# Kernel tuning notes

Hardware: AMD Instinct MI355X
Metric: run time of the kernel (lower is better)

The kernel has to match this reference:

```python
import jax, jax.numpy as jnp
import numpy as np

B, N, E = 8, 1024, 512
H, D = 8, 64
F = 2048


def setup_inputs() -> dict:
    key = jax.random.key(0)
    ks = jax.random.split(key, 12)
    s = lambda *sh: 1.0 / np.sqrt(sh[-1])
    inp = {
        "input1": jax.random.normal(ks[0], (B, N, E), dtype=jnp.float32),
        # projection weights stored as [in, out] (torch weight transposed)
        "Wq": jax.random.normal(ks[1], (E, H * D), dtype=jnp.float32) * s(E, E),
        "Wk": jax.random.normal(ks[2], (E, H * D), dtype=jnp.float32) * s(E, E),
        "Wv": jax.random.normal(ks[3], (E, H * D), dtype=jnp.float32) * s(E, E),
        "Wo": jax.random.normal(ks[4], (H * D, E), dtype=jnp.float32) * s(E, E),
        "bo": jnp.zeros((E,), dtype=jnp.float32),
        "g1": jnp.ones((E,), dtype=jnp.float32),
        "b1": jnp.zeros((E,), dtype=jnp.float32),
        "W1": jax.random.normal(ks[5], (E, F), dtype=jnp.float32) * s(E, E),
        "bf1": jnp.zeros((F,), dtype=jnp.float32),
        "W2": jax.random.normal(ks[6], (F, E), dtype=jnp.float32) * s(F, F),
        "bf2": jnp.zeros((E,), dtype=jnp.float32),
        "g2": jnp.ones((E,), dtype=jnp.float32),
        "b2": jnp.zeros((E,), dtype=jnp.float32),
    }
    return inp


def _layernorm(x, g, b, eps=1e-5):
    mu = jnp.mean(x, axis=-1, keepdims=True)
    var = jnp.var(x, axis=-1, keepdims=True)
    return (x - mu) * jax.lax.rsqrt(var + eps) * g + b


def reference(input1, Wq, Wk, Wv, Wo, bo, g1, b1, W1, bf1, W2, bf2, g2, b2):
    x = input1
    # QKV projections, split heads: [B, H, N, D]
    q = (x @ Wq).reshape(B, N, H, D).transpose(0, 2, 1, 3)
    k = (x @ Wk).reshape(B, N, H, D).transpose(0, 2, 1, 3)
    v = (x @ Wv).reshape(B, N, H, D).transpose(0, 2, 1, 3)
    # scaled dot-product attention (naive, materialized scores as in source)
    score = jnp.einsum("bhnd,bhmd->bhnm", q, k) / jnp.sqrt(jnp.float32(D))
    weights = jax.nn.softmax(score, axis=-1)
    out = jnp.einsum("bhnm,bhmd->bhnd", weights, v)
    out_concat = out.transpose(0, 2, 1, 3).reshape(B, N, H * D)
    mh = out_concat @ Wo + bo
    out1 = _layernorm(x + mh, g1, b1)
    ff = jax.nn.relu(out1 @ W1 + bf1) @ W2 + bf2
    out3 = _layernorm(out1 + ff, g2, b2)
    return (out3, 0)
```

## Files before the change

kernel.cpp:

```cpp
#include <hip/hip_runtime.h>
#include <cstdint>
#include <cstddef>

typedef _Float16 h8 __attribute__((ext_vector_type(8)));
typedef _Float16 h4 __attribute__((ext_vector_type(4)));
typedef __fp16   g2 __attribute__((ext_vector_type(2)));
typedef float    f32x4 __attribute__((ext_vector_type(4)));

constexpr int B_ = 8, N_ = 1024, E_ = 512, H_ = 8, D_ = 64, F_ = 2048;
constexpr int M_ = B_ * N_;
constexpr int HD_ = H_ * D_;

#define QSCALE2 0.18033688011112042f

#define GLOAD_LDS16(gp, lp)                                                        \
    __builtin_amdgcn_global_load_lds((const __attribute__((address_space(1))) void*)(gp), \
                                     (__attribute__((address_space(3))) void*)(lp), 16, 0, 0)

__device__ __forceinline__ float exp2_raw(float x) {
#if __has_builtin(__builtin_amdgcn_exp2f)
    return __builtin_amdgcn_exp2f(x);
#else
    float r;
    asm("v_exp_f32 %0, %1\n\ts_nop 0" : "=v"(r) : "v"(x));
    return r;
#endif
}

__global__ void __launch_bounds__(256) k_pre(
    const float* __restrict__ x, _Float16* __restrict__ xh,
    const float* __restrict__ Wq, const float* __restrict__ Wk,
    const float* __restrict__ Wv, const float* __restrict__ Wo,
    const float* __restrict__ W1, const float* __restrict__ W2,
    _Float16* __restrict__ oqkv, _Float16* __restrict__ oo,
    _Float16* __restrict__ o1, _Float16* __restrict__ o2) {
    if (blockIdx.z == 12) {
        int i = (blockIdx.x * 256 + threadIdx.x) * 16;
#pragma unroll
        for (int j = 0; j < 4; ++j) {
            float4 v = *(const float4*)(x + i + j * 4);
            h4 o = {(_Float16)v.x, (_Float16)v.y, (_Float16)v.z, (_Float16)v.w};
            *(h4*)(xh + i + j * 4) = o;
        }
        return;
    }
    if (blockIdx.x >= 256) return;
    const float* in;
    _Float16* out;
    int R, C, gt = blockIdx.x;
    switch (blockIdx.z) {
        case 0: in = Wq; out = oqkv;              R = 512;  C = 512;  break;
        case 1: in = Wk; out = oqkv + 512 * 512;  R = 512;  C = 512;  break;
        case 2: in = Wv; out = oqkv + 1024 * 512; R = 512;  C = 512;  break;
        case 3: in = Wo; out = oo;                R = 512;  C = 512;  break;
        default:
            if (blockIdx.z < 8) { in = W1; out = o1; R = 512;  C = 2048; gt += (blockIdx.z - 4) * 256; }
            else                { in = W2; out = o2; R = 2048; C = 512;  gt += (blockIdx.z - 8) * 256; }
    }
    const int ctiles = C >> 5;
    const int ty = gt / ctiles, tx = gt - ty * ctiles;
    const int r0 = ty * 32, c0 = tx * 32;
    __shared__ float lt[32][33];
    const int rr = threadIdx.x >> 3, cq = threadIdx.x & 7;
    float4 v = *(const float4*)&in[(size_t)(r0 + rr) * C + c0 + cq * 4];
    lt[rr][cq * 4 + 0] = v.x; lt[rr][cq * 4 + 1] = v.y;
    lt[rr][cq * 4 + 2] = v.z; lt[rr][cq * 4 + 3] = v.w;
    __syncthreads();
    h4 o = {(_Float16)lt[cq * 4 + 0][rr], (_Float16)lt[cq * 4 + 1][rr],
            (_Float16)lt[cq * 4 + 2][rr], (_Float16)lt[cq * 4 + 3][rr]};
    *(h4*)&out[(size_t)(c0 + rr) * R + r0 + cq * 4] = o;
}

template <int BN, int EPI>
__global__ void __launch_bounds__(256) k_gemm(
    const _Float16* __restrict__ A, const _Float16* __restrict__ Bt,
    int Mg, int Ng, int Kg,
    const float* __restrict__ bias,
    const _Float16* __restrict__ resh, _Float16* __restrict__ outh,
    _Float16* __restrict__ qp, _Float16* __restrict__ kp, _Float16* __restrict__ vtp) {
    constexpr int WN = BN / 2;
    constexpr int NI = WN / 16;
    __shared__ alignas(16) _Float16 lA[2][64 * 64];
    __shared__ alignas(16) _Float16 lB[2][BN * 64];

    const int tid = threadIdx.x;
    const int lane = tid & 63;
    const int wid = tid >> 6;
    const int wr = wid >> 1, wc = wid & 1;
    const int r16 = lane & 15, hseg = lane >> 4;

    const int bid = blockIdx.x;
    const int xcd = bid & 7;
    const int rem = bid >> 3;
    const int tx = rem >> 4, tyl = rem & 15;
    const int m0 = (xcd * 16 + tyl) * 64;
    const int n0 = tx * BN;

    auto STAGE = [&](int buf, int k0) {
#pragma unroll
        for (int i = 0; i < 2; ++i) {
            const int slot = i * 256 + tid, row = slot >> 3;
            const int cs = (slot & 7) ^ (row & 7);
            GLOAD_LDS16(A + (size_t)(m0 + row) * Kg + k0 + cs * 8, &lA[buf][slot * 8]);
        }
#pragma unroll
        for (int i = 0; i < BN / 32; ++i) {
            const int slot = i * 256 + tid, row = slot >> 3;
            const int cs = (slot & 7) ^ (row & 7);
            GLOAD_LDS16(Bt + (size_t)(n0 + row) * Kg + k0 + cs * 8, &lB[buf][slot * 8]);
        }
    };

    f32x4 acc[2][NI] = {};
    const int nt = Kg >> 6;

    STAGE(0, 0);
    __syncthreads();

    for (int t = 0; t < nt; ++t) {
        const int cur = t & 1;
        if (t + 1 < nt) STAGE(cur ^ 1, (t + 1) << 6);

#pragma unroll
        for (int kk = 0; kk < 2; ++kk) {
            h8 af[2], bf[NI];
#pragma unroll
            for (int mi = 0; mi < 2; ++mi) {
                const int row = wr * 32 + mi * 16 + r16;
                af[mi] = *(const h8*)&lA[cur][row * 64 + (((kk * 4 + hseg) ^ (row & 7)) * 8)];
            }
#pragma unroll
            for (int ni = 0; ni < NI; ++ni) {
                const int row = wc * WN + ni * 16 + r16;
                bf[ni] = *(const h8*)&lB[cur][row * 64 + (((kk * 4 + hseg) ^ (row & 7)) * 8)];
            }
#pragma unroll
            for (int mi = 0; mi < 2; ++mi)
#pragma unroll
                for (int ni = 0; ni < NI; ++ni)
                    acc[mi][ni] =
                        __builtin_amdgcn_mfma_f32_16x16x32_f16(af[mi], bf[ni], acc[mi][ni], 0, 0, 0);
        }
        __syncthreads();
    }

    if constexpr (EPI == 0) {
        if (n0 >= 1024) {
            _Float16* lC = &lA[0][0];
#pragma unroll
            for (int mi = 0; mi < 2; ++mi) {
                const int r0 = wr * 32 + mi * 16 + hseg * 4;
                const int s = r0 >> 3, ro = r0 & 7;
#pragma unroll
                for (int ni = 0; ni < NI; ++ni) {
                    const int c = wc * WN + ni * 16 + r16;
                    h4 pv = {(_Float16)acc[mi][ni][0], (_Float16)acc[mi][ni][1],
                             (_Float16)acc[mi][ni][2], (_Float16)acc[mi][ni][3]};
                    *(h4*)&lC[c * 64 + ((s ^ (c & 7)) << 3) + ro] = pv;
                }
            }
            __syncthreads();
            const int c = tid >> 1, half = tid & 1;
            const int b = m0 >> 10, nn0 = m0 & 1023;
            _Float16* gdst =
                vtp + ((size_t)(b * 512 + (n0 - 1024) + c)) * 1024 + nn0 + half * 32;
#pragma unroll
            for (int j = 0; j < 4; ++j) {
                const int s = half * 4 + j;
                h8 v = *(const h8*)&lC[c * 64 + ((s ^ (c & 7)) << 3)];
                *(h8*)&gdst[j * 8] = v;
            }
        } else {
#pragma unroll
            for (int mi = 0; mi < 2; ++mi)
#pragma unroll
                for (int ni = 0; ni < NI; ++ni)
#pragma unroll
                    for (int r = 0; r < 4; ++r) {
                        int row = m0 + wr * 32 + mi * 16 + hseg * 4 + r;
                        int col = n0 + wc * WN + ni * 16 + r16;
                        float v = acc[mi][ni][r];
                        int cc = col & 511;
                        int h = cc >> 6, d = cc & 63;
                        int b = row >> 10, nn = row & 1023;
                        if (col < 512)
                            qp[((b * 8 + h) * 1024 + nn) * 64 + d] = (_Float16)(v * QSCALE2);
                        else
                            kp[((b * 8 + h) * 1024 + nn) * 64 + d] = (_Float16)v;
                    }
        }
    } else {
#pragma unroll
        for (int mi = 0; mi < 2; ++mi)
#pragma unroll
            for (int ni = 0; ni < NI; ++ni)
#pragma unroll
                for (int r = 0; r < 4; ++r) {
                    int row = m0 + wr * 32 + mi * 16 + hseg * 4 + r;
                    int col = n0 + wc * WN + ni * 16 + r16;
                    float v = acc[mi][ni][r] + bias[col];
                    if constexpr (EPI == 3) {
                        v += (float)resh[(size_t)row * Ng + col];
                    } else {
                        v = v > 0.f ? v : 0.f;
                    }
                    outh[(size_t)row * Ng + col] = (_Float16)v;
                }
    }
}

__global__ void __launch_bounds__(512) k_attn(const _Float16* __restrict__ q,
                                              const _Float16* __restrict__ k,
                                              const _Float16* __restrict__ vt,
                                              _Float16* __restrict__ attn) {
    __shared__ alignas(16) _Float16 lK[2][64 * 64];
    __shared__ alignas(16) _Float16 lV[2][64 * 64];
    __shared__ alignas(16) _Float16 lP[8][16 * 64];

    const int tid = threadIdx.x, lane = tid & 63, w = tid >> 6;
    const int bid = blockIdx.x;
    const int xcd = bid & 7, rem = bid >> 3;
    const int bh = xcd * 8 + (rem & 7);
    const int q0 = (rem >> 3) * 128;
    const int r16 = lane & 15, hseg = lane >> 4;
    const size_t base = (size_t)bh * N_ * D_;

    h8 qf0 = *(const h8*)&q[base + (size_t)(q0 + w * 16 + r16) * 64 + hseg * 8];
    h8 qf1 = *(const h8*)&q[base + (size_t)(q0 + w * 16 + r16) * 64 + 32 + hseg * 8];

    const int srow = tid >> 3;
    const int scsrc = (tid & 7) ^ (srow & 7);

    auto STAGE = [&](int buf, int kt) {
        GLOAD_LDS16(k + base + kt * 4096 + srow * 64 + scsrc * 8, &lK[buf][tid * 8]);
        GLOAD_LDS16(vt + base + (size_t)srow * N_ + kt * 64 + scsrc * 8, &lV[buf][tid * 8]);
    };

    float mrun = -1e30f, lrun = 0.f;
    f32x4 oacc[4] = {};

    const char* lKb = (const char*)&lK[0][0];
    const char* lVb = (const char*)&lV[0][0];
    char* lPb = (char*)&lP[0][0] + w * 2048;
    const int swz = r16 & 7;
    const int kb0 = r16 * 128 + ((hseg ^ swz) * 16);
    const int kb1 = r16 * 128 + (((4 + hseg) ^ swz) * 16);
    const int pswz = swz * 8;
    const int prd0 = r16 * 128 + (((hseg * 8) ^ pswz) * 2);
    const int prd1 = r16 * 128 + (((32 + hseg * 8) ^ pswz) * 2);
    const int pwr0 = r16 * 128 + (((0 + hseg * 4) ^ pswz) * 2);
    const int pwr1 = r16 * 128 + (((16 + hseg * 4) ^ pswz) * 2);
    const int pwr2 = r16 * 128 + (((32 + hseg * 4) ^ pswz) * 2);
    const int pwr3 = r16 * 128 + (((48 + hseg * 4) ^ pswz) * 2);

    auto TILE = [&](const int cur, const int kt) __attribute__((always_inline)) {
        if (kt + 1 < N_ / 64) STAGE(cur ^ 1, kt + 1);
        const int cOff = cur * 8192;

        float sv[4][4];
        __builtin_amdgcn_s_setprio(1);
#pragma unroll
        for (int t4 = 0; t4 < 4; ++t4) {
            f32x4 a = {};
            h8 kf0 = *(const h8*)(lKb + cOff + t4 * 2048 + kb0);
            a = __builtin_amdgcn_mfma_f32_16x16x32_f16(kf0, qf0, a, 0, 0, 0);
            h8 kf1 = *(const h8*)(lKb + cOff + t4 * 2048 + kb1);
            a = __builtin_amdgcn_mfma_f32_16x16x32_f16(kf1, qf1, a, 0, 0, 0);
#pragma unroll
            for (int r = 0; r < 4; ++r) sv[t4][r] = a[r];
        }
        __builtin_amdgcn_s_setprio(0);

        float m0a = fmaxf(fmaxf(sv[0][0], sv[0][1]), fmaxf(sv[0][2], sv[0][3]));
        float m1a = fmaxf(fmaxf(sv[1][0], sv[1][1]), fmaxf(sv[1][2], sv[1][3]));
        float m2a = fmaxf(fmaxf(sv[2][0], sv[2][1]), fmaxf(sv[2][2], sv[2][3]));
        float m3a = fmaxf(fmaxf(sv[3][0], sv[3][1]), fmaxf(sv[3][2], sv[3][3]));
        float mx = fmaxf(fmaxf(m0a, m1a), fmaxf(m2a, m3a));

        if (__any(mx > mrun + 8.f)) {
            mx = fmaxf(mx, __shfl_xor(mx, 16));
            mx = fmaxf(mx, __shfl_xor(mx, 32));
            float mnew = fmaxf(mrun, mx);
            float sc = exp2_raw(mrun - mnew);
            mrun = mnew;
            lrun *= sc;
#pragma unroll
            for (int r = 0; r < 4; ++r) {
                float scq = __shfl(sc, hseg * 4 + r);
#pragma unroll
                for (int nf = 0; nf < 4; ++nf) oacc[nf][r] *= scq;
            }
        }

        float p[4][4];
        float rsum = 0.f;
#pragma unroll
        for (int t4 = 0; t4 < 4; ++t4)
#pragma unroll
            for (int r = 0; r < 4; ++r) {
                p[t4][r] = exp2_raw(sv[t4][r] - mrun);
                rsum += p[t4][r];
            }
        lrun += rsum;

#pragma unroll
        for (int t4 = 0; t4 < 4; ++t4) {
            g2 a0 = __builtin_amdgcn_cvt_pkrtz(p[t4][0], p[t4][1]);
            g2 a1 = __builtin_amdgcn_cvt_pkrtz(p[t4][2], p[t4][3]);
            h4 pv = {(_Float16)a0[0], (_Float16)a0[1], (_Float16)a1[0], (_Float16)a1[1]};
            char* dst = lPb + (t4 == 0 ? pwr0 : t4 == 1 ? pwr1 : t4 == 2 ? pwr2 : pwr3);
            *(h4*)dst = pv;
        }
        asm volatile("s_waitcnt lgkmcnt(0)" ::: "memory");

        h8 pa0 = *(const h8*)(lPb + prd0);
        h8 pa1 = *(const h8*)(lPb + prd1);
        __builtin_amdgcn_s_setprio(1);
#pragma unroll
        for (int nf = 0; nf < 4; ++nf) {
            h8 vb0 = *(const h8*)(lVb + cOff + nf * 2048 + kb0);
            oacc[nf] = __builtin_amdgcn_mfma_f32_16x16x32_f16(pa0, vb0, oacc[nf], 0, 0, 0);
            h8 vb1 = *(const h8*)(lVb + cOff + nf * 2048 + kb1);
            oacc[nf] = __builtin_amdgcn_mfma_f32_16x16x32_f16(pa1, vb1, oacc[nf], 0, 0, 0);
        }
        __builtin_amdgcn_s_setprio(0);
        __syncthreads();
    };

    STAGE(0, 0);
    __syncthreads();

    for (int kt = 0; kt < N_ / 64; kt += 2) {
        TILE(0, kt);
        TILE(1, kt + 1);
    }

    lrun += __shfl_xor(lrun, 16);
    lrun += __shfl_xor(lrun, 32);

    float rlin = 1.f / lrun;
    int b = bh >> 3, h = bh & 7;
#pragma unroll
    for (int r = 0; r < 4; ++r) {
        float inv = __shfl(rlin, hseg * 4 + r);
        int row = b * 1024 + q0 + w * 16 + hseg * 4 + r;
#pragma unroll
        for (int nf = 0; nf < 4; ++nf) {
            int col = h * 64 + nf * 16 + r16;
            attn[(size_t)row * 512 + col] = (_Float16)(oacc[nf][r] * inv);
        }
    }
}

template <int OUTF32>
__global__ void __launch_bounds__(256) k_ln(const _Float16* __restrict__ x,
                                            const float* __restrict__ g,
                                            const float* __restrict__ b,
                                            float* __restrict__ outf,
                                            _Float16* __restrict__ outh,
                                            float* __restrict__ tail) {
    int row = blockIdx.x * 4 + (threadIdx.x >> 6);
    int lane = threadIdx.x & 63;
    h8 v = *(const h8*)(x + (size_t)row * 512 + lane * 8);
    float f[8];
    float s = 0.f, sq = 0.f;
#pragma unroll
    for (int j = 0; j < 8; ++j) {
        f[j] = (float)v[j];
        s += f[j];
        sq += f[j] * f[j];
    }
#pragma unroll
    for (int msk = 1; msk < 64; msk <<= 1) {
        s += __shfl_xor(s, msk);
        sq += __shfl_xor(sq, msk);
    }
    float mu = s * (1.f / 512.f);
    float var = sq * (1.f / 512.f) - mu * mu;
    float rstd = rsqrtf(var + 1e-5f);
    float4 ga = *(const float4*)(g + lane * 8);
    float4 gb = *(const float4*)(g + lane * 8 + 4);
    float4 ba = *(const float4*)(b + lane * 8);
    float4 bb = *(const float4*)(b + lane * 8 + 4);
    float o[8];
    o[0] = (f[0] - mu) * rstd * ga.x + ba.x;
    o[1] = (f[1] - mu) * rstd * ga.y + ba.y;
    o[2] = (f[2] - mu) * rstd * ga.z + ba.z;
    o[3] = (f[3] - mu) * rstd * ga.w + ba.w;
    o[4] = (f[4] - mu) * rstd * gb.x + bb.x;
    o[5] = (f[5] - mu) * rstd * gb.y + bb.y;
    o[6] = (f[6] - mu) * rstd * gb.z + bb.z;
    o[7] = (f[7] - mu) * rstd * gb.w + bb.w;
    if constexpr (OUTF32) {
        float* orow = outf + (size_t)row * 512 + lane * 8;
        *(float4*)(orow) = make_float4(o[0], o[1], o[2], o[3]);
        *(float4*)(orow + 4) = make_float4(o[4], o[5], o[6], o[7]);
        if (tail && blockIdx.x == 0 && threadIdx.x == 0) tail[0] = 0.f;
    } else {
        h8 oh = {(_Float16)o[0], (_Float16)o[1], (_Float16)o[2], (_Float16)o[3],
                 (_Float16)o[4], (_Float16)o[5], (_Float16)o[6], (_Float16)o[7]};
        *(h8*)(outh + (size_t)row * 512 + lane * 8) = oh;
    }
}

extern "C" void kernel_launch(void* const* d_in, const int* in_sizes, int n_in,
                              void* d_out, int out_size, void* d_ws, size_t ws_size,
                              hipStream_t stream) {
    const float* x   = (const float*)d_in[0];
    const float* Wq  = (const float*)d_in[1];
    const float* Wk  = (const float*)d_in[2];
    const float* Wv  = (const float*)d_in[3];
    const float* Wo  = (const float*)d_in[4];
    const float* bo  = (const float*)d_in[5];
    const float* g1  = (const float*)d_in[6];
    const float* b1  = (const float*)d_in[7];
    const float* W1  = (const float*)d_in[8];
    const float* bf1 = (const float*)d_in[9];
    const float* W2  = (const float*)d_in[10];
    const float* bf2 = (const float*)d_in[11];
    const float* g2  = (const float*)d_in[12];
    const float* b2  = (const float*)d_in[13];
    float* out = (float*)d_out;

    char* ws = (char*)d_ws;
    _Float16* xh    = (_Float16*)(ws + 0);
    _Float16* wqkvT = (_Float16*)(ws + 8388608);
    _Float16* woT   = (_Float16*)(ws + 9961472);
    _Float16* w1T   = (_Float16*)(ws + 10485760);
    _Float16* w2T   = (_Float16*)(ws + 12582912);
    _Float16* qb    = (_Float16*)(ws + 14680064);
    _Float16* kb    = (_Float16*)(ws + 23068672);
    _Float16* vtb   = (_Float16*)(ws + 31457280);
    _Float16* attnb = (_Float16*)(ws + 39845888);
    _Float16* h1h   = (_Float16*)(ws + 48234496);
    _Float16* out1h = xh;
    _Float16* ff    = qb;

    k_pre<<<dim3(1024, 1, 13), 256, 0, stream>>>(x, xh, Wq, Wk, Wv, Wo, W1, W2,
                                                 wqkvT, woT, w1T, w2T);

    k_gemm<128, 0><<<dim3(1536), 256, 0, stream>>>(
        xh, wqkvT, M_, 1536, 512, nullptr, nullptr, nullptr, qb, kb, vtb);

    k_attn<<<dim3(512), 512, 0, stream>>>(qb, kb, vtb, attnb);

    k_gemm<64, 3><<<dim3(1024), 256, 0, stream>>>(
        attnb, woT, M_, 512, 512, bo, xh, h1h, nullptr, nullptr, nullptr);

    k_ln<0><<<dim3(M_ / 4), 256, 0, stream>>>(h1h, g1, b1, nullptr, out1h, nullptr);

    k_gemm<128, 2><<<dim3(2048), 256, 0, stream>>>(
        out1h, w1T, M_, 2048, 512, bf1, nullptr, ff, nullptr, nullptr, nullptr);

    k_gemm<64, 3><<<dim3(1024), 256, 0, stream>>>(
        ff, w2T, M_, 512, 2048, bf2, out1h, h1h, nullptr, nullptr, nullptr);

    k_ln<1><<<dim3(M_ / 4), 256, 0, stream>>>(h1h, g2, b2, out, nullptr, out + (size_t)M_ * E_);
}
```

Measured before the change: 144.4 us.

## Add dedicated 128x64-tile GEMM with 8 waves for N=512 residual GEMMs

```diff
diff --git a/kernel.cpp b/kernel.cpp
--- a/kernel.cpp
+++ b/kernel.cpp
@@ -71,13 +71,14 @@
     *(h4*)&out[(size_t)(c0 + rr) * R + r0 + cq * 4] = o;
 }
 
-template <int BN, int EPI>
+template <int EPI>
 __global__ void __launch_bounds__(256) k_gemm(
     const _Float16* __restrict__ A, const _Float16* __restrict__ Bt,
     int Mg, int Ng, int Kg,
     const float* __restrict__ bias,
-    const _Float16* __restrict__ resh, _Float16* __restrict__ outh,
+    _Float16* __restrict__ outh,
     _Float16* __restrict__ qp, _Float16* __restrict__ kp, _Float16* __restrict__ vtp) {
+    constexpr int BN = 128;
     constexpr int WN = BN / 2;
     constexpr int NI = WN / 16;
     __shared__ alignas(16) _Float16 lA[2][64 * 64];
@@ -199,14 +200,92 @@
                     int row = m0 + wr * 32 + mi * 16 + hseg * 4 + r;
                     int col = n0 + wc * WN + ni * 16 + r16;
                     float v = acc[mi][ni][r] + bias[col];
-                    if constexpr (EPI == 3) {
-                        v += (float)resh[(size_t)row * Ng + col];
-                    } else {
-                        v = v > 0.f ? v : 0.f;
-                    }
+                    v = v > 0.f ? v : 0.f;
                     outh[(size_t)row * Ng + col] = (_Float16)v;
                 }
     }
+}
+
+__global__ void __launch_bounds__(512) k_gemm64(
+    const _Float16* __restrict__ A, const _Float16* __restrict__ Bt,
+    int Ng, int Kg,
+    const float* __restrict__ bias,
+    const _Float16* __restrict__ resh, _Float16* __restrict__ outh) {
+    __shared__ alignas(16) _Float16 lA[2][128 * 64];
+    __shared__ alignas(16) _Float16 lB[2][64 * 64];
+
+    const int tid = threadIdx.x;
+    const int lane = tid & 63;
+    const int wid = tid >> 6;
+    const int wr = wid >> 1;
+    const int wc = wid & 1;
+    const int r16 = lane & 15, hseg = lane >> 4;
+
+    const int bid = blockIdx.x;
+    const int xcd = bid & 7;
+    const int rem = bid >> 3;
+    const int tx = rem >> 3, tyl = rem & 7;
+    const int m0 = (xcd * 8 + tyl) * 128;
+    const int n0 = tx * 64;
+
+    auto STAGE = [&](int buf, int k0) {
+#pragma unroll
+        for (int i = 0; i < 2; ++i) {
+            const int slot = i * 512 + tid, row = slot >> 3;
+            const int cs = (slot & 7) ^ (row & 7);
+            GLOAD_LDS16(A + (size_t)(m0 + row) * Kg + k0 + cs * 8, &lA[buf][slot * 8]);
+        }
+        {
+            const int slot = tid, row = slot >> 3;
+            const int cs = (slot & 7) ^ (row & 7);
+            GLOAD_LDS16(Bt + (size_t)(n0 + row) * Kg + k0 + cs * 8, &lB[buf][slot * 8]);
+        }
+    };
+
+    f32x4 acc[2][2] = {};
+    const int nt = Kg >> 6;
+
+    STAGE(0, 0);
+    __syncthreads();
+
+    for (int t = 0; t < nt; ++t) {
+        const int cur = t & 1;
+        if (t + 1 < nt) STAGE(cur ^ 1, (t + 1) << 6);
+
+#pragma unroll
+        for (int kk = 0; kk < 2; ++kk) {
+            h8 af[2], bf[2];
+#pragma unroll
+            for (int mi = 0; mi < 2; ++mi) {
+                const int row = wr * 32 + mi * 16 + r16;
+                af[mi] = *(const h8*)&lA[cur][row * 64 + (((kk * 4 + hseg) ^ (row & 7)) * 8)];
+            }
+#pragma unroll
+            for (int ni = 0; ni < 2; ++ni) {
+                const int row = wc * 32 + ni * 16 + r16;
+                bf[ni] = *(const h8*)&lB[cur][row * 64 + (((kk * 4 + hseg) ^ (row & 7)) * 8)];
+            }
+#pragma unroll
+            for (int mi = 0; mi < 2; ++mi)
+#pragma unroll
+                for (int ni = 0; ni < 2; ++ni)
+                    acc[mi][ni] =
+                        __builtin_amdgcn_mfma_f32_16x16x32_f16(af[mi], bf[ni], acc[mi][ni], 0, 0, 0);
+        }
+        __syncthreads();
+    }
+
+#pragma unroll
+    for (int mi = 0; mi < 2; ++mi)
+#pragma unroll
+        for (int ni = 0; ni < 2; ++ni)
+#pragma unroll
+            for (int r = 0; r < 4; ++r) {
+                int row = m0 + wr * 32 + mi * 16 + hseg * 4 + r;
+                int col = n0 + wc * 32 + ni * 16 + r16;
+                float v = acc[mi][ni][r] + bias[col] + (float)resh[(size_t)row * Ng + col];
+                outh[(size_t)row * Ng + col] = (_Float16)v;
+            }
 }
 
 __global__ void __launch_bounds__(512) k_attn(const _Float16* __restrict__ q,
@@ -439,21 +518,19 @@
     k_pre<<<dim3(1024, 1, 13), 256, 0, stream>>>(x, xh, Wq, Wk, Wv, Wo, W1, W2,
                                                  wqkvT, woT, w1T, w2T);
 
-    k_gemm<128, 0><<<dim3(1536), 256, 0, stream>>>(
-        xh, wqkvT, M_, 1536, 512, nullptr, nullptr, nullptr, qb, kb, vtb);
+    k_gemm<0><<<dim3(1536), 256, 0, stream>>>(
+        xh, wqkvT, M_, 1536, 512, nullptr, nullptr, qb, kb, vtb);
 
     k_attn<<<dim3(512), 512, 0, stream>>>(qb, kb, vtb, attnb);
 
-    k_gemm<64, 3><<<dim3(1024), 256, 0, stream>>>(
-        attnb, woT, M_, 512, 512, bo, xh, h1h, nullptr, nullptr, nullptr);
+    k_gemm64<<<dim3(512), 512, 0, stream>>>(attnb, woT, 512, 512, bo, xh, h1h);
 
     k_ln<0><<<dim3(M_ / 4), 256, 0, stream>>>(h1h, g1, b1, nullptr, out1h, nullptr);
 
-    k_gemm<128, 2><<<dim3(2048), 256, 0, stream>>>(
-        out1h, w1T, M_, 2048, 512, bf1, nullptr, ff, nullptr, nullptr, nullptr);
-
-    k_gemm<64, 3><<<dim3(1024), 256, 0, stream>>>(
-        ff, w2T, M_, 512, 2048, bf2, out1h, h1h, nullptr, nullptr, nullptr);
+    k_gemm<2><<<dim3(2048), 256, 0, stream>>>(
+        out1h, w1T, M_, 2048, 512, bf1, ff, nullptr, nullptr, nullptr);
+
+    k_gemm64<<<dim3(512), 512, 0, stream>>>(ff, w2T, 512, 2048, bf2, out1h, h1h);
 
     k_ln<1><<<dim3(M_ / 4), 256, 0, stream>>>(h1h, g2, b2, out, nullptr, out + (size_t)M_ * E_);
 }
```

Result: no change. 144.6 us (+0.1%).
